# Performance work log

Hardware: AMD Instinct MI355X
Metric: run time of the kernel (lower is better)

Reference implementation:

```python
import jax, jax.numpy as jnp
import numpy as np

N, C, H, K, HID = 131072, 256, 8, 128, 1024
SCALE = (C // H) ** -0.5  # 1/sqrt(32)


def layernorm(x, g, b, eps=1e-5):
    mu = jnp.mean(x, axis=-1, keepdims=True)
    var = jnp.var(x, axis=-1, keepdims=True)
    return (x - mu) * jax.lax.rsqrt(var + eps) * g + b


def setup_inputs() -> dict:
    key = jax.random.key(0)
    ks = jax.random.split(key, 8)
    feat = jax.random.normal(ks[0], (N, C), dtype=jnp.float32)
    order = jax.random.permutation(ks[1], N)  # serialized order (gather)
    inverse = jnp.argsort(order)              # scatter back (unpad identity)
    s = 0.02
    return {
        "feat": feat,
        "ln1_g": jnp.ones((C,), jnp.float32), "ln1_b": jnp.zeros((C,), jnp.float32),
        "w_qkv": jax.random.normal(ks[2], (C, 3 * C), jnp.float32) * s,
        "b_qkv": jnp.zeros((3 * C,), jnp.float32),
        "w_proj": jax.random.normal(ks[3], (C, C), jnp.float32) * s,
        "b_proj": jnp.zeros((C,), jnp.float32),
        "ln2_g": jnp.ones((C,), jnp.float32), "ln2_b": jnp.zeros((C,), jnp.float32),
        "w1": jax.random.normal(ks[4], (C, HID), jnp.float32) * s,
        "b1": jnp.zeros((HID,), jnp.float32),
        "w2": jax.random.normal(ks[5], (HID, C), jnp.float32) * s,
        "b2": jnp.zeros((C,), jnp.float32),
        "order": order,
        "inverse": inverse,
    }


def attention(x, w_qkv, b_qkv, w_proj, b_proj, order, inverse):
    D = C // H
    qkv = x @ w_qkv + b_qkv                       # [N, 3C]
    qkv = qkv[order]                              # gather to serialized order
    qkv = qkv.reshape(-1, K, 3, H, D)             # [P, K, 3, H, D]
    q, k, v = jnp.moveaxis(qkv, 2, 0)             # each [P, K, H, D]
    q = jnp.swapaxes(q, 1, 2)                     # [P, H, K, D]
    k = jnp.swapaxes(k, 1, 2)
    v = jnp.swapaxes(v, 1, 2)
    attn = jnp.einsum("phkd,phjd->phkj", q * SCALE, k)  # [P, H, K, K]
    attn = jax.nn.softmax(attn, axis=-1)
    out = jnp.einsum("phkj,phjd->phkd", attn, v)  # [P, H, K, D]
    out = jnp.swapaxes(out, 1, 2).reshape(-1, C)  # [N, C]
    out = out[inverse]                            # scatter back to input order
    return out @ w_proj + b_proj


def reference(feat, ln1_g, ln1_b, w_qkv, b_qkv, w_proj, b_proj,
              ln2_g, ln2_b, w1, b1, w2, b2, order, inverse):
    # pre-norm transformer block: x + attn(ln1(x)); x + mlp(ln2(x))
    x = feat
    x = x + attention(layernorm(x, ln1_g, ln1_b), w_qkv, b_qkv, w_proj, b_proj, order, inverse)
    h = layernorm(x, ln2_g, ln2_b)
    h = jax.nn.gelu(h @ w1 + b1) @ w2 + b2
    return x + h
```

## Files before the change

### kernel.cpp

```cpp
#include <hip/hip_runtime.h>
#include <hip/hip_bf16.h>

typedef __hip_bfloat16 bf16;
typedef __bf16 bf16x8 __attribute__((ext_vector_type(8)));
typedef float f32x4 __attribute__((ext_vector_type(4)));

#define N_TOK 131072
#define C_DIM 256
#define HID_DIM 1024

__device__ __forceinline__ void async_copy16(void* lds, const void* g) {
  __builtin_amdgcn_global_load_lds(
      (const __attribute__((address_space(1))) void*)g,
      (__attribute__((address_space(3))) void*)lds, 16, 0, 0);
}

__device__ __forceinline__ float fast_rcp(float x) {
#if __has_builtin(__builtin_amdgcn_rcpf)
  return __builtin_amdgcn_rcpf(x);
#else
  return 1.f / x;
#endif
}

__device__ __forceinline__ bf16 bf16_rne(float f) {
  unsigned u = __float_as_uint(f);
  u += 0x7FFF + ((u >> 16) & 1);
  unsigned short s = (unsigned short)(u >> 16);
  return *reinterpret_cast<bf16*>(&s);
}

__device__ __forceinline__ float fast_gelu(float x) {
  float t = x * x;
  float u = __builtin_fmaf(0.07135481627f, t, 1.5957691216f);
  float z = x * u;
  float e = __expf(-z);
  return x * fast_rcp(1.f + e);
}

__global__ void ln_bf16_kernel(const float* __restrict__ x,
                               const float* __restrict__ g,
                               const float* __restrict__ b,
                               bf16* __restrict__ out) {
  int row = blockIdx.x * 4 + threadIdx.y;
  int lane = threadIdx.x;
  size_t base = (size_t)row * C_DIM + lane * 4;
  float4 v = *(const float4*)(x + base);
  float s = v.x + v.y + v.z + v.w;
  float s2 = v.x * v.x + v.y * v.y + v.z * v.z + v.w * v.w;
#pragma unroll
  for (int m = 1; m < 64; m <<= 1) { s += __shfl_xor(s, m); s2 += __shfl_xor(s2, m); }
  float mean = s * (1.f / 256.f);
  float var = s2 * (1.f / 256.f) - mean * mean;
  float rstd = rsqrtf(var + 1e-5f);
  float4 gv = *(const float4*)(g + lane * 4);
  float4 bv = *(const float4*)(b + lane * 4);
  union { bf16 h[4]; uint2 u; } pk;
  pk.h[0] = bf16_rne((v.x - mean) * rstd * gv.x + bv.x);
  pk.h[1] = bf16_rne((v.y - mean) * rstd * gv.y + bv.y);
  pk.h[2] = bf16_rne((v.z - mean) * rstd * gv.z + bv.z);
  pk.h[3] = bf16_rne((v.w - mean) * rstd * gv.w + bv.w);
  *(uint2*)(out + base) = pk.u;
}

__global__ void cast_transpose_kernel(const float* __restrict__ in, bf16* __restrict__ out,
                                      int K, int N) {
  int idx = blockIdx.x * 256 + threadIdx.x;
  if (idx >= K * N) return;
  int n = idx / K, k = idx - n * K;
  out[idx] = bf16_rne(in[(size_t)k * N + n]);
}

template <int EPI, int NXT>
__global__ __launch_bounds__(256) void gemm_bt_kernel(
    const bf16* __restrict__ A, const bf16* __restrict__ Bt,
    const float* __restrict__ bias, const float* __restrict__ res,
    void* __restrict__ outp, int K, int ldn) {
  __shared__ bf16 sA[128 * 64];
  __shared__ bf16 sB[128 * 64];
  const int bid = blockIdx.x;
  const int xcd = bid & 7;
  const int j = bid >> 3;
  const int n0 = (j % NXT) * 128;
  const int m0 = ((j / NXT) * 8 + xcd) * 128;
  const int tid = threadIdx.x;
  const int wid = tid >> 6;
  const int lane = tid & 63;
  const int quad = lane >> 4;
  const int l16 = lane & 15;
  const int wm = (wid >> 1) * 64;
  const int wn = (wid & 1) * 64;
  const int srow = tid >> 3;
  const int scol = ((tid & 7) ^ (srow & 7)) * 8;

  const bf16* pA = A + (size_t)(m0 + srow) * K + scol;
  const bf16* pB = Bt + (size_t)(n0 + srow) * K + scol;
  const size_t isStride = (size_t)32 * K;

  f32x4 acc[4][4] = {};

  for (int k0 = 0; k0 < K; k0 += 64) {
#pragma unroll
    for (int is = 0; is < 4; ++is) {
      async_copy16(&sA[is * 2048 + wid * 512], pA + is * isStride);
      async_copy16(&sB[is * 2048 + wid * 512], pB + is * isStride);
    }
    pA += 64;
    pB += 64;
    __syncthreads();
#pragma unroll
    for (int kk = 0; kk < 64; kk += 32) {
      bf16x8 af[4], bfr[4];
#pragma unroll
      for (int i = 0; i < 4; ++i)
        af[i] = *(const bf16x8*)&sA[(wm + i * 16 + l16) * 64 +
                                    ((((kk >> 3) + quad) ^ (l16 & 7)) << 3)];
#pragma unroll
      for (int j2 = 0; j2 < 4; ++j2)
        bfr[j2] = *(const bf16x8*)&sB[(wn + j2 * 16 + l16) * 64 +
                                      ((((kk >> 3) + quad) ^ (l16 & 7)) << 3)];
#pragma unroll
      for (int i = 0; i < 4; ++i)
#pragma unroll
        for (int j2 = 0; j2 < 4; ++j2)
          acc[i][j2] = __builtin_amdgcn_mfma_f32_16x16x32_bf16(af[i], bfr[j2], acc[i][j2], 0, 0, 0);
    }
    __syncthreads();
  }

  float bv[4];
#pragma unroll
  for (int j2 = 0; j2 < 4; ++j2) bv[j2] = bias[n0 + wn + j2 * 16 + l16];
  const int colb = n0 + wn + l16;
#pragma unroll
  for (int i = 0; i < 4; ++i) {
    int rowb = m0 + wm + i * 16 + quad * 4;
#pragma unroll
    for (int r = 0; r < 4; ++r) {
      size_t rowoff = (size_t)(rowb + r) * ldn + colb;
#pragma unroll
      for (int j2 = 0; j2 < 4; ++j2) {
        size_t idx = rowoff + j2 * 16;
        float v = acc[i][j2][r] + bv[j2];
        if constexpr (EPI == 0) {
          ((bf16*)outp)[idx] = bf16_rne(v);
        } else if constexpr (EPI == 1) {
          ((float*)outp)[idx] = v + res[idx];
        } else if constexpr (EPI == 2) {
          ((bf16*)outp)[idx] = bf16_rne(fast_gelu(v));
        } else {
          ((float*)outp)[idx] = v + res[idx];
        }
      }
    }
  }
}

__global__ __launch_bounds__(256) void attn_kernel(
    const bf16* __restrict__ qkv, const int* __restrict__ order,
    bf16* __restrict__ outw) {
  __shared__ bf16 sK[128 * 40];
  __shared__ bf16 sVt[32 * 136];
  __shared__ bf16 sP[128 * 136];
  __shared__ int sOrd[128];
  const int bid = blockIdx.x;
  const int h = (bid >> 3) & 7;
  const int p = ((bid >> 6) << 3) | (bid & 7);
  const int tid = threadIdx.x;
  const int wid = tid >> 6;
  const int lane = tid & 63;
  const int quad = lane >> 4;
  const int l16 = lane & 15;

  if (tid < 128) sOrd[tid] = order[p * 128 + tid];
  __syncthreads();

  {
    int r = tid >> 1;
    int half = (tid & 1) * 16;
    size_t base = (size_t)sOrd[r] * 768 + h * 32;
    uint4 ka = *(const uint4*)&qkv[base + 256 + half];
    uint4 kb = *(const uint4*)&qkv[base + 256 + half + 8];
    *(uint4*)&sK[r * 40 + half] = ka;
    *(uint4*)&sK[r * 40 + half + 8] = kb;
    union { uint4 u[2]; bf16 e[16]; } vv;
    vv.u[0] = *(const uint4*)&qkv[base + 512 + half];
    vv.u[1] = *(const uint4*)&qkv[base + 512 + half + 8];
#pragma unroll
    for (int c = 0; c < 16; ++c) sVt[(half + c) * 136 + r] = vv.e[c];
  }
  __syncthreads();

  bf16x8 qf[2];
#pragma unroll
  for (int t = 0; t < 2; ++t) {
    int r = wid * 32 + t * 16 + l16;
    qf[t] = *(const bf16x8*)&qkv[(size_t)sOrd[r] * 768 + h * 32 + quad * 8];
  }

  const f32x4 zero = {0.f, 0.f, 0.f, 0.f};
  f32x4 s[2][8];
#pragma unroll
  for (int ct = 0; ct < 8; ++ct) {
    bf16x8 kf = *(const bf16x8*)&sK[(ct * 16 + l16) * 40 + quad * 8];
#pragma unroll
    for (int t = 0; t < 2; ++t)
      s[t][ct] = __builtin_amdgcn_mfma_f32_16x16x32_bf16(qf[t], kf, zero, 0, 0, 0);
  }

  const float scale = 0.17677669529663687f;
#pragma unroll
  for (int t = 0; t < 2; ++t) {
#pragma unroll
    for (int r = 0; r < 4; ++r) {
      float mx = -1e30f;
#pragma unroll
      for (int ct = 0; ct < 8; ++ct) mx = fmaxf(mx, s[t][ct][r]);
      mx *= scale;
#pragma unroll
      for (int mk = 1; mk < 16; mk <<= 1) mx = fmaxf(mx, __shfl_xor(mx, mk));
      float sum = 0.f;
#pragma unroll
      for (int ct = 0; ct < 8; ++ct) {
        float e = __expf(scale * s[t][ct][r] - mx);
        s[t][ct][r] = e;
        sum += e;
      }
#pragma unroll
      for (int mk = 1; mk < 16; mk <<= 1) sum += __shfl_xor(sum, mk);
      float inv = fast_rcp(sum);
      int prow = wid * 32 + t * 16 + quad * 4 + r;
#pragma unroll
      for (int ct = 0; ct < 8; ++ct)
        sP[prow * 136 + ct * 16 + l16] = bf16_rne(s[t][ct][r] * inv);
    }
  }
  __syncthreads();

  f32x4 o[2][2] = {};
#pragma unroll
  for (int ks = 0; ks < 4; ++ks) {
    bf16x8 vf[2];
#pragma unroll
    for (int n = 0; n < 2; ++n)
      vf[n] = *(const bf16x8*)&sVt[(n * 16 + l16) * 136 + ks * 32 + quad * 8];
#pragma unroll
    for (int t = 0; t < 2; ++t) {
      bf16x8 pf = *(const bf16x8*)&sP[(wid * 32 + t * 16 + l16) * 136 + ks * 32 + quad * 8];
#pragma unroll
      for (int n = 0; n < 2; ++n)
        o[t][n] = __builtin_amdgcn_mfma_f32_16x16x32_bf16(pf, vf[n], o[t][n], 0, 0, 0);
    }
  }

#pragma unroll
  for (int t = 0; t < 2; ++t) {
    int rowb = wid * 32 + t * 16 + quad * 4;
#pragma unroll
    for (int r = 0; r < 4; ++r) {
      size_t gbase = (size_t)sOrd[rowb + r] * 256 + h * 32;
#pragma unroll
      for (int n = 0; n < 2; ++n)
        outw[gbase + n * 16 + l16] = bf16_rne(o[t][n][r]);
    }
  }
}

extern "C" void kernel_launch(void* const* d_in, const int* in_sizes, int n_in,
                              void* d_out, int out_size, void* d_ws, size_t ws_size,
                              hipStream_t stream) {
  const float* feat   = (const float*)d_in[0];
  const float* ln1_g  = (const float*)d_in[1];
  const float* ln1_b  = (const float*)d_in[2];
  const float* w_qkv  = (const float*)d_in[3];
  const float* b_qkv  = (const float*)d_in[4];
  const float* w_proj = (const float*)d_in[5];
  const float* b_proj = (const float*)d_in[6];
  const float* ln2_g  = (const float*)d_in[7];
  const float* ln2_b  = (const float*)d_in[8];
  const float* w1     = (const float*)d_in[9];
  const float* b1     = (const float*)d_in[10];
  const float* w2     = (const float*)d_in[11];
  const float* b2     = (const float*)d_in[12];
  const int* order    = (const int*)d_in[13];
  float* out = (float*)d_out;

  char* ws = (char*)d_ws;
  size_t off = 0;
  auto take = [&](size_t bytes) {
    char* pp = ws + off;
    off += (bytes + 255) & ~(size_t)255;
    return pp;
  };
  bf16* ln_buf  = (bf16*)take((size_t)N_TOK * 256 * 2);
  bf16* qkv     = (bf16*)take((size_t)N_TOK * 768 * 2);
  bf16* attn_o  = (bf16*)take((size_t)N_TOK * 256 * 2);
  float* xres   = (float*)take((size_t)N_TOK * 256 * 4);
  bf16* wqkvT   = (bf16*)take(768 * 256 * 2);
  bf16* wprojT  = (bf16*)take(256 * 256 * 2);
  bf16* w1T     = (bf16*)take(1024 * 256 * 2);
  bf16* w2T     = (bf16*)take(256 * 1024 * 2);
  bf16* hbuf    = qkv;

  cast_transpose_kernel<<<768, 256, 0, stream>>>(w_qkv, wqkvT, 256, 768);
  cast_transpose_kernel<<<256, 256, 0, stream>>>(w_proj, wprojT, 256, 256);
  cast_transpose_kernel<<<1024, 256, 0, stream>>>(w1, w1T, 256, 1024);
  cast_transpose_kernel<<<1024, 256, 0, stream>>>(w2, w2T, 1024, 256);

  ln_bf16_kernel<<<N_TOK / 4, dim3(64, 4), 0, stream>>>(feat, ln1_g, ln1_b, ln_buf);
  gemm_bt_kernel<0, 6><<<6 * 1024, 256, 0, stream>>>(ln_buf, wqkvT, b_qkv, nullptr, qkv, 256, 768);
  attn_kernel<<<8 * 1024, 256, 0, stream>>>(qkv, order, attn_o);
  gemm_bt_kernel<1, 2><<<2 * 1024, 256, 0, stream>>>(attn_o, wprojT, b_proj, feat, xres, 256, 256);
  ln_bf16_kernel<<<N_TOK / 4, dim3(64, 4), 0, stream>>>(xres, ln2_g, ln2_b, ln_buf);
  gemm_bt_kernel<2, 8><<<8 * 1024, 256, 0, stream>>>(ln_buf, w1T, b1, nullptr, hbuf, 256, 1024);
  gemm_bt_kernel<3, 2><<<2 * 1024, 256, 0, stream>>>(hbuf, w2T, b2, xres, out, 1024, 256);
}
```

Before: 832.6 us.

## Double-buffer GEMM LDS tiles with 64-row M tiles and compile-time K

The GEMM kernel now keeps two LDS buffers and issues async global-to-LDS loads for the next K step before computing the current one, so memory latency overlaps with MFMA work. Each block's M tile shrinks from 128 to 64 rows, which doubles the grid, and K becomes a template constant so the step loop can be fully unrolled. The goal is to hide load latency and improve occupancy. In exchange, A-tile reuse per block drops and B tiles are loaded twice as often overall.

```diff
diff --git a/kernel.cpp b/kernel.cpp
--- a/kernel.cpp
+++ b/kernel.cpp
@@ -71,61 +71,75 @@
   out[idx] = bf16_rne(in[(size_t)k * N + n]);
 }
 
-template <int EPI, int NXT>
+template <int EPI, int NXT, int NSTEP>
 __global__ __launch_bounds__(256) void gemm_bt_kernel(
     const bf16* __restrict__ A, const bf16* __restrict__ Bt,
     const float* __restrict__ bias, const float* __restrict__ res,
-    void* __restrict__ outp, int K, int ldn) {
-  __shared__ bf16 sA[128 * 64];
-  __shared__ bf16 sB[128 * 64];
+    void* __restrict__ outp, int ldn) {
+  constexpr int K = NSTEP * 64;
+  __shared__ bf16 sA[2][64 * 64];
+  __shared__ bf16 sB[2][128 * 64];
   const int bid = blockIdx.x;
   const int xcd = bid & 7;
   const int j = bid >> 3;
   const int n0 = (j % NXT) * 128;
-  const int m0 = ((j / NXT) * 8 + xcd) * 128;
+  const int m0 = ((j / NXT) * 8 + xcd) * 64;
   const int tid = threadIdx.x;
   const int wid = tid >> 6;
   const int lane = tid & 63;
   const int quad = lane >> 4;
   const int l16 = lane & 15;
-  const int wm = (wid >> 1) * 64;
-  const int wn = (wid & 1) * 64;
+  const int wm = (wid & 1) * 32;
+  const int wn = (wid >> 1) * 64;
   const int srow = tid >> 3;
   const int scol = ((tid & 7) ^ (srow & 7)) * 8;
 
   const bf16* pA = A + (size_t)(m0 + srow) * K + scol;
   const bf16* pB = Bt + (size_t)(n0 + srow) * K + scol;
-  const size_t isStride = (size_t)32 * K;
-
-  f32x4 acc[4][4] = {};
-
-  for (int k0 = 0; k0 < K; k0 += 64) {
-#pragma unroll
-    for (int is = 0; is < 4; ++is) {
-      async_copy16(&sA[is * 2048 + wid * 512], pA + is * isStride);
-      async_copy16(&sB[is * 2048 + wid * 512], pB + is * isStride);
-    }
-    pA += 64;
-    pB += 64;
-    __syncthreads();
+  const size_t rs = (size_t)32 * K;
+
+  async_copy16(&sA[0][0 * 2048 + wid * 512], pA);
+  async_copy16(&sA[0][1 * 2048 + wid * 512], pA + rs);
+#pragma unroll
+  for (int is = 0; is < 4; ++is)
+    async_copy16(&sB[0][is * 2048 + wid * 512], pB + is * rs);
+  pA += 64;
+  pB += 64;
+
+  f32x4 acc[2][4] = {};
+
+#pragma unroll
+  for (int s = 0; s < NSTEP; ++s) {
+    asm volatile("s_waitcnt vmcnt(0) lgkmcnt(0)\n\ts_barrier" ::: "memory");
+    if (s + 1 < NSTEP) {
+      const int nb = (s + 1) & 1;
+      async_copy16(&sA[nb][0 * 2048 + wid * 512], pA);
+      async_copy16(&sA[nb][1 * 2048 + wid * 512], pA + rs);
+#pragma unroll
+      for (int is = 0; is < 4; ++is)
+        async_copy16(&sB[nb][is * 2048 + wid * 512], pB + is * rs);
+      pA += 64;
+      pB += 64;
+    }
+    const bf16* a_s = sA[s & 1];
+    const bf16* b_s = sB[s & 1];
 #pragma unroll
     for (int kk = 0; kk < 64; kk += 32) {
-      bf16x8 af[4], bfr[4];
-#pragma unroll
-      for (int i = 0; i < 4; ++i)
-        af[i] = *(const bf16x8*)&sA[(wm + i * 16 + l16) * 64 +
-                                    ((((kk >> 3) + quad) ^ (l16 & 7)) << 3)];
+      bf16x8 af[2], bfr[4];
+#pragma unroll
+      for (int i = 0; i < 2; ++i)
+        af[i] = *(const bf16x8*)&a_s[(wm + i * 16 + l16) * 64 +
+                                     ((((kk >> 3) + quad) ^ (l16 & 7)) << 3)];
 #pragma unroll
       for (int j2 = 0; j2 < 4; ++j2)
-        bfr[j2] = *(const bf16x8*)&sB[(wn + j2 * 16 + l16) * 64 +
-                                      ((((kk >> 3) + quad) ^ (l16 & 7)) << 3)];
-#pragma unroll
-      for (int i = 0; i < 4; ++i)
+        bfr[j2] = *(const bf16x8*)&b_s[(wn + j2 * 16 + l16) * 64 +
+                                       ((((kk >> 3) + quad) ^ (l16 & 7)) << 3)];
+#pragma unroll
+      for (int i = 0; i < 2; ++i)
 #pragma unroll
         for (int j2 = 0; j2 < 4; ++j2)
           acc[i][j2] = __builtin_amdgcn_mfma_f32_16x16x32_bf16(af[i], bfr[j2], acc[i][j2], 0, 0, 0);
     }
-    __syncthreads();
   }
 
   float bv[4];
@@ -133,7 +147,7 @@
   for (int j2 = 0; j2 < 4; ++j2) bv[j2] = bias[n0 + wn + j2 * 16 + l16];
   const int colb = n0 + wn + l16;
 #pragma unroll
-  for (int i = 0; i < 4; ++i) {
+  for (int i = 0; i < 2; ++i) {
     int rowb = m0 + wm + i * 16 + quad * 4;
 #pragma unroll
     for (int r = 0; r < 4; ++r) {
@@ -308,10 +322,10 @@
   cast_transpose_kernel<<<1024, 256, 0, stream>>>(w2, w2T, 1024, 256);
 
   ln_bf16_kernel<<<N_TOK / 4, dim3(64, 4), 0, stream>>>(feat, ln1_g, ln1_b, ln_buf);
-  gemm_bt_kernel<0, 6><<<6 * 1024, 256, 0, stream>>>(ln_buf, wqkvT, b_qkv, nullptr, qkv, 256, 768);
+  gemm_bt_kernel<0, 6, 4><<<6 * 2048, 256, 0, stream>>>(ln_buf, wqkvT, b_qkv, nullptr, qkv, 768);
   attn_kernel<<<8 * 1024, 256, 0, stream>>>(qkv, order, attn_o);
-  gemm_bt_kernel<1, 2><<<2 * 1024, 256, 0, stream>>>(attn_o, wprojT, b_proj, feat, xres, 256, 256);
+  gemm_bt_kernel<1, 2, 4><<<2 * 2048, 256, 0, stream>>>(attn_o, wprojT, b_proj, feat, xres, 256);
   ln_bf16_kernel<<<N_TOK / 4, dim3(64, 4), 0, stream>>>(xres, ln2_g, ln2_b, ln_buf);
-  gemm_bt_kernel<2, 8><<<8 * 1024, 256, 0, stream>>>(ln_buf, w1T, b1, nullptr, hbuf, 256, 1024);
-  gemm_bt_kernel<3, 2><<<2 * 1024, 256, 0, stream>>>(hbuf, w2T, b2, xres, out, 1024, 256);
-}
+  gemm_bt_kernel<2, 8, 4><<<8 * 2048, 256, 0, stream>>>(ln_buf, w1T, b1, nullptr, hbuf, 1024);
+  gemm_bt_kernel<3, 2, 16><<<2 * 2048, 256, 0, stream>>>(hbuf, w2T, b2, xres, out, 256);
+}
```

Measured after the change: 873.6 us. +4.9%, slower.
